# Optimization experiments

Measured on AMD Instinct MI355X. Metric: run time of the kernel, lower is better.

Reference implementation:

```python
import jax, jax.numpy as jnp
import numpy as np

N, E = 100000, 400000
IN_CH, OUT_CH, HEADS, TIME_DIM, MSG_DIM = 100, 100, 2, 100, 100
EDGE_DIM = MSG_DIM + TIME_DIM  # 200
MEAN_DT, STD_DT = 0.0, 1.0


def setup_inputs() -> dict:
    key = jax.random.key(0)
    ks = jax.random.split(key, 16)
    HC = HEADS * OUT_CH
    s_in = 1.0 / np.sqrt(IN_CH)
    s_e = 1.0 / np.sqrt(EDGE_DIM)
    return {
        "x": jax.random.normal(ks[0], (N, IN_CH), jnp.float32),
        "last_update": jax.random.uniform(ks[1], (N,), jnp.float32) * 1000.0,
        "edge_index": jax.random.randint(ks[2], (2, E), 0, N, jnp.int32),
        "t": jax.random.uniform(ks[3], (E,), jnp.float32) * 1000.0,
        "msg": jax.random.normal(ks[4], (E, MSG_DIM), jnp.float32),
        "w_time": jax.random.normal(ks[5], (TIME_DIM,), jnp.float32),
        "b_time": jax.random.normal(ks[6], (TIME_DIM,), jnp.float32) * 0.1,
        "Wq": jax.random.normal(ks[7], (IN_CH, HC), jnp.float32) * s_in,
        "bq": jnp.zeros((HC,), jnp.float32),
        "Wk": jax.random.normal(ks[8], (IN_CH, HC), jnp.float32) * s_in,
        "bk": jnp.zeros((HC,), jnp.float32),
        "Wv": jax.random.normal(ks[9], (IN_CH, HC), jnp.float32) * s_in,
        "bv": jnp.zeros((HC,), jnp.float32),
        "We": jax.random.normal(ks[10], (EDGE_DIM, HC), jnp.float32) * s_e,  # lin_edge (no bias in PyG)
        "Ws": jax.random.normal(ks[11], (IN_CH, HC), jnp.float32) * s_in,   # lin_skip (root weight)
        "bs": jnp.zeros((HC,), jnp.float32),
    }


def reference(x, last_update, edge_index, t, msg, w_time, b_time,
              Wq, bq, Wk, bk, Wv, bv, We, Ws, bs):
    n = x.shape[0]
    src, dst = edge_index[0], edge_index[1]
    # relative time encoding: cos(Linear(1 -> TIME_DIM))
    rel_t = jnp.abs(last_update[src] - t)
    rel_t = (rel_t - MEAN_DT) / STD_DT
    t_enc = jnp.cos(rel_t[:, None] * w_time[None, :] + b_time)  # [E, TIME_DIM]
    edge_attr = jnp.concatenate([t_enc, msg], axis=-1)          # [E, EDGE_DIM]

    # TransformerConv (heads=2, concat=True, root_weight=True; dropout off in eval)
    q = (x @ Wq + bq).reshape(n, HEADS, OUT_CH)                 # [N,H,C]
    k = ((x @ Wk + bk)[src]).reshape(-1, HEADS, OUT_CH)         # [E,H,C]
    v = ((x @ Wv + bv)[src]).reshape(-1, HEADS, OUT_CH)
    e = (edge_attr @ We).reshape(-1, HEADS, OUT_CH)
    k = k + e
    v = v + e

    alpha = jnp.einsum('ehc,ehc->eh', q[dst], k) / np.sqrt(OUT_CH)  # [E,H]
    # segment softmax over incoming edges of each dst node
    amax = jax.ops.segment_max(alpha, dst, num_segments=n)          # [N,H]
    ex = jnp.exp(alpha - amax[dst])
    denom = jax.ops.segment_sum(ex, dst, num_segments=n)            # [N,H]
    attn = ex / (denom[dst] + 1e-16)                                # [E,H]

    out = jax.ops.segment_sum(v * attn[..., None], dst, num_segments=n)  # [N,H,C]
    out = out.reshape(n, HEADS * OUT_CH) + (x @ Ws + bs)
    return out
```

## Files before the change

kernel.cpp:

```cpp
#include <hip/hip_runtime.h>
#include <math.h>

#define N_NODES 100000
#define N_EDGES 400000
#define IN_CH   100
#define OUT_CH  100
#define HEADS   2
#define HC      200
#define TIME_DIM 100
#define MSG_DIM  100
#define EDGE_DIM 200
#define KP_NODE 128
#define KP_EDGE 224
#define NP_EDGE 208
#define PAD_HC  256
#define EW      264
#define NSLAB_ELEMS (13 * 16 * KP_NODE)
#define W4T_ELEMS   (4 * NSLAB_ELEMS)
#define M_CHUNK 128
#define NCHUNK  782

typedef __attribute__((ext_vector_type(8))) short bf16x8_t;
typedef __attribute__((ext_vector_type(4))) float f32x4_t;

struct __align__(8) us4 { unsigned short x, y, z, w; };

static __device__ __forceinline__ float b2f(unsigned short u){
  union { float f; unsigned int i; } v; v.i = ((unsigned int)u) << 16; return v.f;
}
static __device__ __forceinline__ unsigned short f2b(float f){
  union { float f; unsigned int i; } v; v.f = f;
  unsigned int x = v.i;
  return (unsigned short)((x + 0x7fffu + ((x >> 16) & 1u)) >> 16);
}

static __device__ __forceinline__ float fast_cos(float x){
  float r = x * 0.15915494309189535f;
  r = __builtin_amdgcn_fractf(r);
  return __builtin_amdgcn_cosf(r);
}

#define LDS_FENCE() do { \
  asm volatile("s_waitcnt lgkmcnt(0)" ::: "memory"); \
  __builtin_amdgcn_sched_barrier(0); \
} while (0)

__global__ __launch_bounds__(256) void pack_weights(
    const float* __restrict__ Wq, const float* __restrict__ bq,
    const float* __restrict__ Wk, const float* __restrict__ bk,
    const float* __restrict__ Wv, const float* __restrict__ bv,
    const float* __restrict__ We, const float* __restrict__ Ws, const float* __restrict__ bs,
    unsigned short* __restrict__ W4T, unsigned short* __restrict__ WeT,
    float* __restrict__ bias4)
{
  int idx = blockIdx.x * 256 + threadIdx.x;
  if (idx < W4T_ELEMS) {
    int row = idx >> 7;
    int k   = idx & 127;
    int t = row >> 4, j = row & 15;
    int slab = t / 13, i = t % 13;
    int col = i * 16 + j;
    float v = 0.f;
    if (k < IN_CH && col < HC) {
      const float* W = (slab == 0) ? Wq : (slab == 1) ? Wk : (slab == 2) ? Wv : Ws;
      v = W[k * HC + col];
    }
    W4T[idx] = f2b(v);
    return;
  }
  int j = idx - W4T_ELEMS;
  if (j < NP_EDGE * KP_EDGE) {
    int n = j / KP_EDGE, k = j % KP_EDGE;
    float v = 0.f;
    if (n < HC && k < EDGE_DIM) v = We[k * HC + n];
    WeT[j] = f2b(v);
    return;
  }
  j -= NP_EDGE * KP_EDGE;
  if (j < 4 * 208) {
    int slab = j / 208, col = j % 208;
    const float* B = (slab == 0) ? bq : (slab == 1) ? bk : (slab == 2) ? bv : bs;
    bias4[j] = (col < HC) ? B[col] : 0.f;
  }
}

__global__ __launch_bounds__(256) void node_gemm(
    const float* __restrict__ x, const unsigned short* __restrict__ W4T,
    const float* __restrict__ bias4,
    unsigned short* __restrict__ q_b, unsigned short* __restrict__ k_b,
    unsigned short* __restrict__ v_b, float* __restrict__ out)
{
  __shared__ __align__(16) unsigned char smem[34816];
  unsigned short* xt = (unsigned short*)smem;

  const int tid   = threadIdx.x;
  const int slab  = blockIdx.x & 3;
  const int chunk = blockIdx.x >> 2;
  const int n0    = chunk * M_CHUNK;
  const int nrows = (N_NODES - n0 < M_CHUNK) ? (N_NODES - n0) : M_CHUNK;

  const int lane = tid & 63, wave = tid >> 6;
  const int m16 = lane & 15, quad = lane >> 4;
  const int rb = wave * 32;

  for (int idx = lane; idx < 800; idx += 64) {
    int r = idx / 25, j = (idx % 25) * 4;
    int gr = rb + r;
    unsigned short* dst = xt + gr * 136 + j;
    if (gr < nrows) {
      float4 xv = *reinterpret_cast<const float4*>(x + (size_t)(n0 + gr) * IN_CH + j);
      dst[0] = f2b(xv.x); dst[1] = f2b(xv.y); dst[2] = f2b(xv.z); dst[3] = f2b(xv.w);
    } else {
      us4 z = {0, 0, 0, 0};
      *reinterpret_cast<us4*>(dst) = z;
    }
  }
  for (int idx = lane; idx < 224; idx += 64) {
    int r = idx / 7, j = idx % 7;
    us4 z = {0, 0, 0, 0};
    *reinterpret_cast<us4*>(&xt[(rb + r) * 136 + 100 + j * 4]) = z;
  }
  LDS_FENCE();

  float bias_v[13];
  #pragma unroll
  for (int i = 0; i < 13; i++) bias_v[i] = bias4[slab * 208 + i * 16 + m16];

  f32x4_t acc[2][13];
  #pragma unroll
  for (int s = 0; s < 2; s++)
    #pragma unroll
    for (int i = 0; i < 13; i++) acc[s][i] = (f32x4_t){0.f, 0.f, 0.f, 0.f};

  const unsigned short* Wp = W4T + (size_t)slab * NSLAB_ELEMS;
  for (int kc = 0; kc < 4; kc++) {
    bf16x8_t a0 = *reinterpret_cast<const bf16x8_t*>(&xt[(rb + m16) * 136 + kc * 32 + quad * 8]);
    bf16x8_t a1 = *reinterpret_cast<const bf16x8_t*>(&xt[(rb + 16 + m16) * 136 + kc * 32 + quad * 8]);
    #pragma unroll
    for (int i = 0; i < 13; i++) {
      bf16x8_t b = *reinterpret_cast<const bf16x8_t*>(
          &Wp[(size_t)(i * 16 + m16) * KP_NODE + kc * 32 + quad * 8]);
      acc[0][i] = __builtin_amdgcn_mfma_f32_16x16x32_bf16(a0, b, acc[0][i], 0, 0, 0);
      acc[1][i] = __builtin_amdgcn_mfma_f32_16x16x32_bf16(a1, b, acc[1][i], 0, 0, 0);
    }
  }

  unsigned short* stg  = xt + rb * 136;
  float*          stgf = (float*)stg;

  if (slab < 2) {
    unsigned short* gb = (slab == 0) ? q_b : k_b;
    for (int s = 0; s < 2; s++) {
      LDS_FENCE();
      for (int idx = lane; idx < 224; idx += 64) {
        int r = idx / 14, j = idx % 14;
        int col = (j < 7) ? (100 + j * 4) : (228 + (j - 7) * 4);
        us4 z = {0, 0, 0, 0};
        *reinterpret_cast<us4*>(&stg[r * 256 + col]) = z;
      }
      #pragma unroll
      for (int i = 0; i < 13; i++) {
        int c = i * 16 + m16;
        if (c < 200) {
          int pc = (c < 100) ? c : c + 28;
          #pragma unroll
          for (int r = 0; r < 4; r++)
            stg[(quad * 4 + r) * 256 + pc] = f2b(acc[s][i][r] + bias_v[i]);
        }
      }
      LDS_FENCE();
      const int rbase = rb + s * 16;
      uint4* g = (uint4*)(gb + (size_t)(n0 + rbase) * PAD_HC);
      const uint4* sv = (const uint4*)stg;
      for (int idx = lane; idx < 512; idx += 64)
        if (rbase + (idx >> 5) < nrows) g[idx] = sv[idx];
    }
  } else if (slab == 2) {
    for (int s = 0; s < 2; s++) {
      LDS_FENCE();
      #pragma unroll
      for (int i = 0; i < 13; i++) {
        int c = i * 16 + m16;
        if (c < 200) {
          #pragma unroll
          for (int r = 0; r < 4; r++)
            stg[(quad * 4 + r) * 200 + c] = f2b(acc[s][i][r] + bias_v[i]);
        }
      }
      LDS_FENCE();
      const int rbase = rb + s * 16;
      uint4* g = (uint4*)(v_b + (size_t)(n0 + rbase) * HC);
      const uint4* sv = (const uint4*)stg;
      for (int idx = lane; idx < 400; idx += 64)
        if (rbase + idx / 25 < nrows) g[idx] = sv[idx];
    }
  } else {
    for (int r8 = 0; r8 < 4; r8++) {
      const int s = r8 >> 1;
      LDS_FENCE();
      if ((quad >> 1) == (r8 & 1)) {
        int lr = (quad & 1) * 4;
        #pragma unroll
        for (int i = 0; i < 13; i++) {
          int c = i * 16 + m16;
          if (c < 200) {
            #pragma unroll
            for (int r = 0; r < 4; r++)
              stgf[(lr + r) * 200 + c] = acc[s][i][r] + bias_v[i];
          }
        }
      }
      LDS_FENCE();
      const int rbase = rb + r8 * 8;
      uint4* g = (uint4*)(out + (size_t)(n0 + rbase) * HC);
      const uint4* sv = (const uint4*)stgf;
      for (int idx = lane; idx < 400; idx += 64)
        if (rbase + idx / 50 < nrows) g[idx] = sv[idx];
    }
  }
}

__global__ __launch_bounds__(256, 3) void edge_gemm(
    const int* __restrict__ edge_index, const float* __restrict__ t,
    const float* __restrict__ last_update, const float* __restrict__ msg,
    const float* __restrict__ w_time, const float* __restrict__ b_time,
    const unsigned short* __restrict__ WeT,
    const unsigned short* __restrict__ q_b, const unsigned short* __restrict__ k_b,
    const unsigned short* __restrict__ v_b, const int* __restrict__ pos,
    unsigned short* __restrict__ v_e, float* __restrict__ exbuf)
{
  __shared__ __align__(16) unsigned short e_lds[64 * EW];
  __shared__ int   src_s[64], dst_s[64], pos_s[64];
  __shared__ float rel_s[64], wt_s[TIME_DIM], bt_s[TIME_DIM];

  const int tid = threadIdx.x;
  const int e0 = blockIdx.x * 64;

  if (tid < TIME_DIM) { wt_s[tid] = w_time[tid]; bt_s[tid] = b_time[tid]; }
  else if (tid >= 128 && tid < 192) {
    int el = tid - 128; int e = e0 + el;
    int s = edge_index[e], d = edge_index[N_EDGES + e];
    src_s[el] = s; dst_s[el] = d;
    pos_s[el] = pos[e];
    rel_s[el] = fabsf(last_update[s] - t[e]);
  }
  __syncthreads();

  const int lane = tid & 63, wave = tid >> 6;
  const int m16 = lane & 15, quad = lane >> 4;
  const int r0 = wave * 16;
  unsigned short* my = e_lds + r0 * EW;

  const int my_src = src_s[r0 + m16];
  const int my_dst = dst_s[r0 + m16];

  us4 vpre[13];
  #pragma unroll
  for (int j = 0; j < 13; j++) {
    int idx = j * 64 + lane;
    if (idx < 800) {
      int row = idx / 50, c = (idx % 50) * 4;
      vpre[j] = *reinterpret_cast<const us4*>(&v_b[(size_t)src_s[r0 + row] * HC + c]);
    }
  }

  float4 mpre[7];
  #pragma unroll
  for (int j = 0; j < 7; j++) {
    int idx = j * 64 + lane;
    if (idx < 400) {
      int row = idx / 25, c4 = (idx % 25) * 4;
      mpre[j] = *reinterpret_cast<const float4*>(
          msg + (size_t)(e0 + r0 + row) * MSG_DIM + c4);
    }
  }
  #pragma unroll
  for (int j = 0; j < 7; j++) {
    int idx = j * 64 + lane;
    if (idx < 400) {
      int row = idx / 25, c4 = (idx % 25) * 4;
      float rel = rel_s[r0 + row];
      us4 o;
      o.x = f2b(fast_cos(rel * wt_s[c4 + 0] + bt_s[c4 + 0]));
      o.y = f2b(fast_cos(rel * wt_s[c4 + 1] + bt_s[c4 + 1]));
      o.z = f2b(fast_cos(rel * wt_s[c4 + 2] + bt_s[c4 + 2]));
      o.w = f2b(fast_cos(rel * wt_s[c4 + 3] + bt_s[c4 + 3]));
      *reinterpret_cast<us4*>(&my[row * EW + c4]) = o;
    }
  }
  for (int idx = lane; idx < 96; idx += 64) {
    int row = idx / 6, c4 = 200 + (idx % 6) * 4;
    us4 z = {0, 0, 0, 0};
    *reinterpret_cast<us4*>(&my[row * EW + c4]) = z;
  }
  #pragma unroll
  for (int j = 0; j < 7; j++) {
    int idx = j * 64 + lane;
    if (idx < 400) {
      int row = idx / 25, c4 = (idx % 25) * 4;
      us4 o;
      o.x = f2b(mpre[j].x); o.y = f2b(mpre[j].y);
      o.z = f2b(mpre[j].z); o.w = f2b(mpre[j].w);
      *reinterpret_cast<us4*>(&my[row * EW + 100 + c4]) = o;
    }
  }
  __syncthreads();

  f32x4_t acc[4][4];
  #pragma unroll
  for (int i = 0; i < 4; i++)
    #pragma unroll
    for (int m = 0; m < 4; m++) acc[i][m] = (f32x4_t){0.f, 0.f, 0.f, 0.f};

  #pragma unroll
  for (int i = 0; i < 4; i++) {
    const int nt = wave + 4 * i;
    if (nt < 13) {
      for (int kc = 0; kc < 7; kc++) {
        bf16x8_t b = *reinterpret_cast<const bf16x8_t*>(
            &WeT[(nt * 16 + m16) * KP_EDGE + kc * 32 + quad * 8]);
        #pragma unroll
        for (int m = 0; m < 4; m++) {
          bf16x8_t a = *reinterpret_cast<const bf16x8_t*>(
              &e_lds[(m * 16 + m16) * EW + kc * 32 + quad * 8]);
          acc[i][m] = __builtin_amdgcn_mfma_f32_16x16x32_bf16(a, b, acc[i][m], 0, 0, 0);
        }
      }
    }
  }
  __syncthreads();

  #pragma unroll
  for (int i = 0; i < 4; i++) {
    const int nt = wave + 4 * i;
    if (nt < 13) {
      int c = nt * 16 + m16;
      if (c < 200) {
        int pc = (c < 100) ? c : c + 28;
        #pragma unroll
        for (int m = 0; m < 4; m++)
          #pragma unroll
          for (int r = 0; r < 4; r++)
            e_lds[(m * 16 + quad * 4 + r) * EW + pc] = f2b(acc[i][m][r]);
      }
    }
  }
  for (int idx = lane; idx < 224; idx += 64) {
    int row = idx / 14, j = idx % 14;
    int col = (j < 7) ? (100 + j * 4) : (228 + (j - 7) * 4);
    us4 z = {0, 0, 0, 0};
    *reinterpret_cast<us4*>(&my[row * EW + col]) = z;
  }
  __syncthreads();

  f32x4_t dacc[2];
  dacc[0] = (f32x4_t){0.f, 0.f, 0.f, 0.f};
  dacc[1] = (f32x4_t){0.f, 0.f, 0.f, 0.f};
  #pragma unroll
  for (int h = 0; h < 2; h++) {
    #pragma unroll
    for (int kc = 0; kc < 4; kc++) {
      int ko = h * 128 + kc * 32 + quad * 8;
      bf16x8_t a  = *reinterpret_cast<const bf16x8_t*>(&q_b[(size_t)my_dst * PAD_HC + ko]);
      bf16x8_t kb = *reinterpret_cast<const bf16x8_t*>(&k_b[(size_t)my_src * PAD_HC + ko]);
      bf16x8_t eb = *reinterpret_cast<const bf16x8_t*>(&my[m16 * EW + ko]);
      dacc[h] = __builtin_amdgcn_mfma_f32_16x16x32_bf16(a, kb, dacc[h], 0, 0, 0);
      dacc[h] = __builtin_amdgcn_mfma_f32_16x16x32_bf16(a, eb, dacc[h], 0, 0, 0);
    }
  }
  if (quad == (m16 >> 2)) {
    int r = m16 & 3;
    size_t p = (size_t)pos_s[r0 + m16];
    exbuf[p * 2 + 0] = expf(dacc[0][r] * 0.1f);
    exbuf[p * 2 + 1] = expf(dacc[1][r] * 0.1f);
  }

  #pragma unroll
  for (int j = 0; j < 13; j++) {
    int idx = j * 64 + lane;
    if (idx < 800) {
      int row = idx / 50, c = (idx % 50) * 4;
      int pc = (c < 100) ? c : c + 28;
      us4 ev = *reinterpret_cast<const us4*>(&my[row * EW + pc]);
      us4 o;
      o.x = f2b(b2f(ev.x) + b2f(vpre[j].x));
      o.y = f2b(b2f(ev.y) + b2f(vpre[j].y));
      o.z = f2b(b2f(ev.z) + b2f(vpre[j].z));
      o.w = f2b(b2f(ev.w) + b2f(vpre[j].w));
      *reinterpret_cast<us4*>(&v_e[(size_t)pos_s[r0 + row] * HC + c]) = o;
    }
  }
}

__global__ __launch_bounds__(256) void hist_kernel(const int* __restrict__ edge_index,
                                                   int* __restrict__ deg)
{
  int e = blockIdx.x * 256 + threadIdx.x;
  if (e < N_EDGES) atomicAdd(&deg[edge_index[N_EDGES + e]], 1);
}

__global__ __launch_bounds__(256) void scan1(const int* __restrict__ deg,
                                             int* __restrict__ cursor, int* __restrict__ bsum)
{
  __shared__ int s[256];
  const int tid = threadIdx.x;
  const int base = blockIdx.x * 1024 + tid * 4;
  int v[4]; int sum = 0;
  #pragma unroll
  for (int j = 0; j < 4; j++) {
    int i = base + j;
    v[j] = (i < N_NODES) ? deg[i] : 0;
    sum += v[j];
  }
  s[tid] = sum; __syncthreads();
  for (int d = 1; d < 256; d <<= 1) {
    int y = (tid >= d) ? s[tid - d] : 0;
    __syncthreads();
    s[tid] += y;
    __syncthreads();
  }
  int excl = s[tid] - sum;
  if (tid == 255) bsum[blockIdx.x] = s[255];
  int run = excl;
  #pragma unroll
  for (int j = 0; j < 4; j++) {
    int i = base + j;
    if (i < N_NODES) cursor[i] = run;
    run += v[j];
  }
}

__global__ void scan2(int* __restrict__ bsum, int nb)
{
  if (threadIdx.x == 0) {
    int acc = 0;
    for (int i = 0; i < nb; i++) { int t = bsum[i]; bsum[i] = acc; acc += t; }
  }
}

__global__ __launch_bounds__(256) void scan3(int* __restrict__ cursor,
                                             const int* __restrict__ bsum)
{
  int i = blockIdx.x * 256 + threadIdx.x;
  if (i < N_NODES) cursor[i] += bsum[i >> 10];
}

__global__ __launch_bounds__(256) void fill_csr(const int* __restrict__ edge_index,
                                                int* __restrict__ cursor, int* __restrict__ pos)
{
  int e = blockIdx.x * 256 + threadIdx.x;
  if (e < N_EDGES) {
    int p = atomicAdd(&cursor[edge_index[N_EDGES + e]], 1);
    pos[e] = p;
  }
}

__global__ __launch_bounds__(256) void gather_out(
    const int* __restrict__ cursor ,
    const int* __restrict__ deg,
    const unsigned short* __restrict__ v_e, const float* __restrict__ exbuf,
    float* __restrict__ out)
{
  const int wave = threadIdx.x >> 6, lane = threadIdx.x & 63;
  const int n = blockIdx.x * 4 + wave;
  const int dg = deg[n];
  const int off = cursor[n] - dg;

  float d0 = 1e-16f, d1 = 1e-16f;
  const int c0 = lane, c1 = lane + 64, c2 = lane + 128, c3 = lane + 192;
  float a0 = 0.f, a1 = 0.f, a2 = 0.f, a3 = 0.f;
  for (int j = 0; j < dg; j++) {
    size_t p = (size_t)(off + j);
    float ex0 = exbuf[p * 2 + 0];
    float ex1 = exbuf[p * 2 + 1];
    d0 += ex0; d1 += ex1;
    const unsigned short* vr = v_e + p * HC;
    a0 += ((c0 < 100) ? ex0 : ex1) * b2f(vr[c0]);
    a1 += ((c1 < 100) ? ex0 : ex1) * b2f(vr[c1]);
    a2 += ex1 * b2f(vr[c2]);
    if (c3 < HC) a3 += ex1 * b2f(vr[c3]);
  }
  const float i0 = 1.f / d0, i1 = 1.f / d1;
  float* o = out + (size_t)n * HC;
  o[c0] += a0 * ((c0 < 100) ? i0 : i1);
  o[c1] += a1 * ((c1 < 100) ? i0 : i1);
  o[c2] += a2 * i1;
  if (c3 < HC) o[c3] += a3 * i1;
}

extern "C" void kernel_launch(void* const* d_in, const int* in_sizes, int n_in,
                              void* d_out, int out_size, void* d_ws, size_t ws_size,
                              hipStream_t stream)
{
  const float* x           = (const float*)d_in[0];
  const float* last_update = (const float*)d_in[1];
  const int*   edge_index  = (const int*)  d_in[2];
  const float* t           = (const float*)d_in[3];
  const float* msg         = (const float*)d_in[4];
  const float* w_time      = (const float*)d_in[5];
  const float* b_time      = (const float*)d_in[6];
  const float* Wq = (const float*)d_in[7];  const float* bq = (const float*)d_in[8];
  const float* Wk = (const float*)d_in[9];  const float* bk = (const float*)d_in[10];
  const float* Wv = (const float*)d_in[11]; const float* bv = (const float*)d_in[12];
  const float* We = (const float*)d_in[13];
  const float* Ws = (const float*)d_in[14]; const float* bs = (const float*)d_in[15];
  float* out = (float*)d_out;

  char* ws = (char*)d_ws;
  size_t off = 0;
  auto alloc = [&](size_t bytes) -> void* {
    void* p = ws + off;
    off = (off + bytes + 255) & ~(size_t)255;
    return p;
  };
  unsigned short* W4T   = (unsigned short*)alloc((size_t)W4T_ELEMS * 2);
  unsigned short* WeT   = (unsigned short*)alloc((size_t)NP_EDGE * KP_EDGE * 2);
  float*          bias4 = (float*)         alloc((size_t)4 * 208 * 4);
  unsigned short* q_b   = (unsigned short*)alloc((size_t)N_NODES * PAD_HC * 2);
  unsigned short* k_b   = (unsigned short*)alloc((size_t)N_NODES * PAD_HC * 2);
  unsigned short* v_b   = (unsigned short*)alloc((size_t)N_NODES * HC * 2);
  unsigned short* v_e   = (unsigned short*)alloc((size_t)N_EDGES * HC * 2);
  float*          exbuf = (float*)         alloc((size_t)N_EDGES * 2 * 4);
  int*            deg   = (int*)           alloc((size_t)N_NODES * 4);
  int*            cursor= (int*)           alloc((size_t)N_NODES * 4);
  int*            bsum  = (int*)           alloc((size_t)128 * 4);
  int*            pos   = (int*)           alloc((size_t)N_EDGES * 4);

  hipMemsetAsync(deg, 0, (size_t)N_NODES * 4, stream);

  {
    int total = W4T_ELEMS + NP_EDGE * KP_EDGE + 4 * 208;
    pack_weights<<<(total + 255) / 256, 256, 0, stream>>>(
        Wq, bq, Wk, bk, Wv, bv, We, Ws, bs, W4T, WeT, bias4);
  }
  hist_kernel<<<(N_EDGES + 255) / 256, 256, 0, stream>>>(edge_index, deg);
  const int nb = (N_NODES + 1023) / 1024;
  scan1<<<nb, 256, 0, stream>>>(deg, cursor, bsum);
  scan2<<<1, 64, 0, stream>>>(bsum, nb);
  scan3<<<(N_NODES + 255) / 256, 256, 0, stream>>>(cursor, bsum);
  fill_csr<<<(N_EDGES + 255) / 256, 256, 0, stream>>>(edge_index, cursor, pos);

  node_gemm<<<NCHUNK * 4, 256, 0, stream>>>(x, W4T, bias4, q_b, k_b, v_b, out);
  edge_gemm<<<N_EDGES / 64, 256, 0, stream>>>(
      edge_index, t, last_update, msg, w_time, b_time, WeT, q_b, k_b, v_b, pos,
      v_e, exbuf);
  gather_out<<<N_NODES / 4, 256, 0, stream>>>(cursor, deg, v_e, exbuf, out);
}
```

Baseline: 804.2 us.

## Process edges in CSR (dst-sorted) order in edge_gemm via permutation index

New measurement: 778.2 us. 3.2% less time.

```diff
diff --git a/kernel.cpp b/kernel.cpp
--- a/kernel.cpp
+++ b/kernel.cpp
@@ -40,6 +40,12 @@
   return __builtin_amdgcn_cosf(r);
 }
 
+static __device__ __forceinline__ float fast_exp(float x){
+  float r;
+  asm("v_exp_f32 %0, %1" : "=v"(r) : "v"(x * 1.4426950408889634f));
+  return r;
+}
+
 #define LDS_FENCE() do { \
   asm volatile("s_waitcnt lgkmcnt(0)" ::: "memory"); \
   __builtin_amdgcn_sched_barrier(0); \
@@ -107,13 +113,14 @@
     int r = idx / 25, j = (idx % 25) * 4;
     int gr = rb + r;
     unsigned short* dst = xt + gr * 136 + j;
+    us4 o;
     if (gr < nrows) {
       float4 xv = *reinterpret_cast<const float4*>(x + (size_t)(n0 + gr) * IN_CH + j);
-      dst[0] = f2b(xv.x); dst[1] = f2b(xv.y); dst[2] = f2b(xv.z); dst[3] = f2b(xv.w);
+      o.x = f2b(xv.x); o.y = f2b(xv.y); o.z = f2b(xv.z); o.w = f2b(xv.w);
     } else {
-      us4 z = {0, 0, 0, 0};
-      *reinterpret_cast<us4*>(dst) = z;
-    }
+      o.x = o.y = o.z = o.w = 0;
+    }
+    *reinterpret_cast<us4*>(dst) = o;
   }
   for (int idx = lane; idx < 224; idx += 64) {
     int r = idx / 7, j = idx % 7;
@@ -220,17 +227,17 @@
   }
 }
 
-__global__ __launch_bounds__(256, 3) void edge_gemm(
+__global__ __launch_bounds__(256, 4) void edge_gemm(
     const int* __restrict__ edge_index, const float* __restrict__ t,
     const float* __restrict__ last_update, const float* __restrict__ msg,
     const float* __restrict__ w_time, const float* __restrict__ b_time,
     const unsigned short* __restrict__ WeT,
     const unsigned short* __restrict__ q_b, const unsigned short* __restrict__ k_b,
-    const unsigned short* __restrict__ v_b, const int* __restrict__ pos,
+    const unsigned short* __restrict__ v_b, const int* __restrict__ csr,
     unsigned short* __restrict__ v_e, float* __restrict__ exbuf)
 {
   __shared__ __align__(16) unsigned short e_lds[64 * EW];
-  __shared__ int   src_s[64], dst_s[64], pos_s[64];
+  __shared__ int   e_s[64], src_s[64], dst_s[64];
   __shared__ float rel_s[64], wt_s[TIME_DIM], bt_s[TIME_DIM];
 
   const int tid = threadIdx.x;
@@ -238,10 +245,10 @@
 
   if (tid < TIME_DIM) { wt_s[tid] = w_time[tid]; bt_s[tid] = b_time[tid]; }
   else if (tid >= 128 && tid < 192) {
-    int el = tid - 128; int e = e0 + el;
+    int el = tid - 128;
+    int e = csr[e0 + el];
     int s = edge_index[e], d = edge_index[N_EDGES + e];
-    src_s[el] = s; dst_s[el] = d;
-    pos_s[el] = pos[e];
+    e_s[el] = e; src_s[el] = s; dst_s[el] = d;
     rel_s[el] = fabsf(last_update[s] - t[e]);
   }
   __syncthreads();
@@ -271,7 +278,7 @@
     if (idx < 400) {
       int row = idx / 25, c4 = (idx % 25) * 4;
       mpre[j] = *reinterpret_cast<const float4*>(
-          msg + (size_t)(e0 + r0 + row) * MSG_DIM + c4);
+          msg + (size_t)e_s[r0 + row] * MSG_DIM + c4);
     }
   }
   #pragma unroll
@@ -370,9 +377,9 @@
   }
   if (quad == (m16 >> 2)) {
     int r = m16 & 3;
-    size_t p = (size_t)pos_s[r0 + m16];
-    exbuf[p * 2 + 0] = expf(dacc[0][r] * 0.1f);
-    exbuf[p * 2 + 1] = expf(dacc[1][r] * 0.1f);
+    size_t p = (size_t)(e0 + r0 + m16);
+    exbuf[p * 2 + 0] = fast_exp(dacc[0][r] * 0.1f);
+    exbuf[p * 2 + 1] = fast_exp(dacc[1][r] * 0.1f);
   }
 
   #pragma unroll
@@ -387,7 +394,7 @@
       o.y = f2b(b2f(ev.y) + b2f(vpre[j].y));
       o.z = f2b(b2f(ev.z) + b2f(vpre[j].z));
       o.w = f2b(b2f(ev.w) + b2f(vpre[j].w));
-      *reinterpret_cast<us4*>(&v_e[(size_t)pos_s[r0 + row] * HC + c]) = o;
+      *reinterpret_cast<us4*>(&v_e[(size_t)(e0 + r0 + row) * HC + c]) = o;
     }
   }
 }
@@ -446,12 +453,12 @@
 }
 
 __global__ __launch_bounds__(256) void fill_csr(const int* __restrict__ edge_index,
-                                                int* __restrict__ cursor, int* __restrict__ pos)
+                                                int* __restrict__ cursor, int* __restrict__ csr)
 {
   int e = blockIdx.x * 256 + threadIdx.x;
   if (e < N_EDGES) {
     int p = atomicAdd(&cursor[edge_index[N_EDGES + e]], 1);
-    pos[e] = p;
+    csr[p] = e;
   }
 }
 
@@ -524,7 +531,7 @@
   int*            deg   = (int*)           alloc((size_t)N_NODES * 4);
   int*            cursor= (int*)           alloc((size_t)N_NODES * 4);
   int*            bsum  = (int*)           alloc((size_t)128 * 4);
-  int*            pos   = (int*)           alloc((size_t)N_EDGES * 4);
+  int*            csr   = (int*)           alloc((size_t)N_EDGES * 4);
 
   hipMemsetAsync(deg, 0, (size_t)N_NODES * 4, stream);
 
@@ -538,11 +545,11 @@
   scan1<<<nb, 256, 0, stream>>>(deg, cursor, bsum);
   scan2<<<1, 64, 0, stream>>>(bsum, nb);
   scan3<<<(N_NODES + 255) / 256, 256, 0, stream>>>(cursor, bsum);
-  fill_csr<<<(N_EDGES + 255) / 256, 256, 0, stream>>>(edge_index, cursor, pos);
+  fill_csr<<<(N_EDGES + 255) / 256, 256, 0, stream>>>(edge_index, cursor, csr);
 
   node_gemm<<<NCHUNK * 4, 256, 0, stream>>>(x, W4T, bias4, q_b, k_b, v_b, out);
   edge_gemm<<<N_EDGES / 64, 256, 0, stream>>>(
-      edge_index, t, last_update, msg, w_time, b_time, WeT, q_b, k_b, v_b, pos,
+      edge_index, t, last_update, msg, w_time, b_time, WeT, q_b, k_b, v_b, csr,
       v_e, exbuf);
   gather_out<<<N_NODES / 4, 256, 0, stream>>>(cursor, deg, v_e, exbuf, out);
 }
```
